# Kernel optimization log

Hardware: AMD Instinct MI355X
Metric: run time of the kernel (lower is better)

Reference implementation:

```python
import jax, jax.numpy as jnp
import numpy as np

N_STEPS = 5
DT = 0.1
# radius fixed from initial sigma = 0.5 + 4.5*sigmoid(0.5) = 3.301 -> ceil(3*sigma) = 10
RADIUS = 10
SIZE = 2 * RADIUS + 1


def _pad1(x):
    return jnp.pad(x, ((0, 0), (0, 0), (1, 1), (1, 1)), mode='reflect')


def _spatial_gradient(x):
    p = _pad1(x)
    gy = (p[:, :, 2:, 1:-1] - p[:, :, :-2, 1:-1]) / 2.0
    gx = (p[:, :, 1:-1, 2:] - p[:, :, 1:-1, :-2]) / 2.0
    return gy, gx


def _laplacian(x):
    p = _pad1(x)
    return (p[:, :, :-2, 1:-1] + p[:, :, 2:, 1:-1]
            + p[:, :, 1:-1, :-2] + p[:, :, 1:-1, 2:] - 4.0 * x)


def _gaussian_blur(x, sigma):
    # differentiable kernel weights, fixed size (matches torch: radius from detached sigma)
    coords = jnp.arange(SIZE, dtype=x.dtype) - RADIUS
    k = jnp.exp(-coords ** 2 / (2.0 * sigma ** 2 + 1e-8))
    k = k / (k.sum() + 1e-8)
    xp = jnp.pad(x, ((0, 0), (0, 0), (0, 0), (RADIUS, RADIUS)), mode='reflect')
    out = jax.lax.conv_general_dilated(xp, k.reshape(1, 1, 1, SIZE), (1, 1), 'VALID')
    out = jnp.pad(out, ((0, 0), (0, 0), (RADIUS, RADIUS), (0, 0)), mode='reflect')
    out = jax.lax.conv_general_dilated(out, k.reshape(1, 1, SIZE, 1), (1, 1), 'VALID')
    return out


def _forward(image, lfd_map, alpha_raw, lambda_raw, log_sigma, log_beta, log_xi,
             eta_raw, nu_raw, log_gamma, omega_raw):
    sig = jax.nn.sigmoid
    alpha = 0.6 + 1.4 * sig(alpha_raw)
    lam = 0.01 + 0.19 * sig(lambda_raw)
    sigma = 0.5 + 4.5 * sig(log_sigma)
    beta = 1.0 + 4.0 * sig(log_beta)
    xi = 1.0 + 4.0 * sig(log_xi)
    eta = sig(eta_raw)
    nu = sig(nu_raw)
    gamma = 1.0 + 3.0 * sig(log_gamma)
    omega = sig(omega_raw)

    fractal_weight = jnp.clip(1.0 - omega * lfd_map, 0.0, 1.0)  # (B,1,H,W)
    u = image
    u0 = image
    for _ in range(N_STEPS):
        u_sigma = _gaussian_blur(u, sigma)
        gy, gx = _spatial_gradient(u)
        gys, gxs = _spatial_gradient(u_sigma)
        grad_mag = jnp.sqrt(gx ** 2 + gy ** 2 + 1e-8)
        grad_mag_s = jnp.sqrt(gxs ** 2 + gys ** 2 + 1e-8)
        lap_abs = jnp.abs(_laplacian(u))
        # conductance phi(s) = beta*sqrt(xi/(eta*s^2+eps)), clamped at 10
        phi = jnp.minimum(beta * jnp.sqrt(xi / (eta * grad_mag_s ** 2 + 1e-6)), 10.0)
        phi_f = phi * fractal_weight
        # curvature modulation psi'(s) = 1e-4*sqrt(nu*s^3+gamma), s = |grad u|*|lap u|
        s = grad_mag * lap_abs
        psi = 1e-4 * jnp.sqrt(nu * s ** 3 + gamma)
        pu = _pad1(u)
        dn = pu[:, :, :-2, 1:-1] - u
        dso = pu[:, :, 2:, 1:-1] - u
        de = pu[:, :, 1:-1, 2:] - u
        dw = pu[:, :, 1:-1, :-2] - u
        pp = _pad1(phi_f)
        div = (pp[:, :, :-2, 1:-1] * dn + pp[:, :, 2:, 1:-1] * dso
               + pp[:, :, 1:-1, 2:] * de + pp[:, :, 1:-1, :-2] * dw)
        du = alpha * psi * div - lam * (u - u0)
        u = jnp.clip(u + DT * du, 0.0, 1.0)
    edge_residual = jnp.abs(image - u)
    er_max = edge_residual.max(axis=(-2, -1), keepdims=True)
    edge_residual = edge_residual / (er_max + 1e-8)
    return u, edge_residual


def setup_inputs() -> dict:
    key = jax.random.key(0)
    k1, k2 = jax.random.split(key)
    B, H, W = 16, 512, 512
    image = jax.random.uniform(k1, (B, 1, H, W), jnp.float32)
    lfd_map = jax.random.uniform(k2, (B, 1, H, W), jnp.float32)
    f = lambda v: jnp.asarray(v, jnp.float32)
    return {
        'image': image, 'lfd_map': lfd_map,
        'alpha_raw': f(0.0), 'lambda_raw': f(-2.0), 'log_sigma': f(0.5),
        'log_beta': f(0.5), 'log_xi': f(0.5), 'eta_raw': f(0.3),
        'nu_raw': f(0.0), 'log_gamma': f(0.5), 'omega_raw': f(0.5),
    }


def reference(image, lfd_map, alpha_raw, lambda_raw, log_sigma, log_beta, log_xi,
              eta_raw, nu_raw, log_gamma, omega_raw):
    return _forward(image, lfd_map, alpha_raw, lambda_raw, log_sigma, log_beta,
                    log_xi, eta_raw, nu_raw, log_gamma, omega_raw)
```

## Files before the change

kernel.cpp:

```cpp
#include <hip/hip_runtime.h>
#include <math.h>

#define HH 512
#define WW 512
#define NPIX (16*HH*WW)
#define RAD 10
#define KS 21
#define TX 64
#define TY 32
#define SH 42
#define SW 74
#define SSTR 90

__device__ __forceinline__ int refl(int v, int n){ v = v < 0 ? -v : v; return v >= n ? 2*n - 2 - v : v; }
__device__ __forceinline__ float sigm(float x){ return 1.f/(1.f+expf(-x)); }

__global__ void k_params(const float* a_raw, const float* l_raw, const float* lsig,
                         const float* lbeta, const float* lxi, const float* e_raw,
                         const float* n_raw, const float* lgam, const float* o_raw,
                         float* P)
{
    if (threadIdx.x || blockIdx.x) return;
    float sigma = 0.5f + 4.5f*sigm(lsig[0]);
    float beta  = 1.f + 4.f*sigm(lbeta[0]);
    float xi    = 1.f + 4.f*sigm(lxi[0]);
    float eta   = sigm(e_raw[0]);
    P[0] = 0.6f + 1.4f*sigm(a_raw[0]);
    P[1] = 0.01f + 0.19f*sigm(l_raw[0]);
    P[2] = beta;
    P[3] = xi;
    P[4] = eta;
    P[5] = sigm(n_raw[0]);
    P[6] = 1.f + 3.f*sigm(lgam[0]);
    P[7] = sigm(o_raw[0]);
    float kk[KS], s = 0.f;
    for (int i = 0; i < KS; ++i){ float c = (float)(i-RAD); kk[i] = expf(-c*c/(2.f*sigma*sigma+1e-8f)); s += kk[i]; }
    float inv = 1.f/(s+1e-8f);
    for (int i = 0; i < KS; ++i) P[8+i] = kk[i]*inv;
    P[30] = (beta*beta*xi >= 100.f*(eta*0.5000002f + 1e-6f)) ? 1.f : 0.f;
    for (int i = 0; i < 16; ++i) P[64+32*i] = 0.f;
}

#define ROW6(v, S, off) float v##0=(S)[(off)], v##1=(S)[(off)+1], v##2=(S)[(off)+2], \
                              v##3=(S)[(off)+3], v##4=(S)[(off)+4], v##5=(S)[(off)+5];
#define ROW8S(v, S, off) float v##m=(S)[(off)-2], v##0=(S)[(off)], v##1=(S)[(off)+1], v##2=(S)[(off)+2], \
                               v##3=(S)[(off)+3], v##4=(S)[(off)+4], v##5=(S)[(off)+5], v##6=(S)[(off)+7];

__global__ __launch_bounds__(256) __attribute__((amdgpu_waves_per_eu(4, 4)))
void k_mega(const float* __restrict__ img, const float* __restrict__ lfd,
            float* __restrict__ out_u, float* __restrict__ out_r,
            const float* __restrict__ P, float* Pmax)
{
    if (P[30] == 0.f) return;
    __shared__ float SA[SH*SSTR];
    __shared__ float SB[SH*SSTR];
    __shared__ float red[4];
    const int tid = threadIdx.x;
    const bool active = tid < 240;
    const int py = tid / 12;
    const int px = tid - 12*py;
    const int ox = blockIdx.x * TX, oy = blockIdx.y * TY;
    const int b = blockIdx.z;
    const float* ib = img + (b<<18);
    const float* lb = lfd + (b<<18);
    const float A = 1e-3f*P[0], lam = P[1], nu = P[5], gam = P[6], omg = P[7];
    const float nuA = A*A*nu, gamA = A*A*gam;
    const bool bord = (ox == 0) | (oy == 0) | (ox == WW - TX) | (oy == HH - TY);

    for (int i = tid; i < SW*SH; i += 256){
        int r = i / SW, c = i - r*SW;
        int gy = oy - 5 + r, gx = ox - 5 + c;
        if (bord){ gy = refl(gy, HH); gx = refl(gx, WW); }
        int gi = gy*WW + gx;
        int pc = (c == 0) ? 0 : (c + (c-1)/6 + 1);
        SA[r*SSTR + pc] = ib[gi];
        SB[r*SSTR + pc] = fminf(fmaxf(1.f - omg*lb[gi], 0.f), 1.f);
    }
    __syncthreads();

    const int c0 = 1 + 6*px;
    const int r0 = 1 + 2*py;
    const int bi = r0*SSTR + 7*px + 2;

    ROW6(fa, SB, bi-SSTR) ROW8S(fb, SB, bi) ROW8S(fc, SB, bi+SSTR) ROW6(fd, SB, bi+2*SSTR)
    ROW6(zb, SA, bi) ROW6(zc, SA, bi+SSTR)
    __syncthreads();

    float ub0=zb0, ub1=zb1, ub2=zb2, ub3=zb3, ub4=zb4, ub5=zb5;
    float uc0=zc0, uc1=zc1, uc2=zc2, uc3=zc3, uc4=zc4, uc5=zc5;

    auto CF = [&](float cc, float cn, float cs, float cw, float ce,
                  float fn, float fs, float fw_, float fe, float z) -> float {
        float dy = cs - cn, dx = ce - cw;
        float g2 = fmaf(0.25f, fmaf(dy, dy, dx*dx), 1e-8f);
        float t1 = (cn + cs) + (ce + cw);
        float lap = fmaf(-4.f, cc, t1);
        float s = sqrtf(g2) * fabsf(lap);
        float psiA = sqrtf(fmaf(nuA, s*s*s, gamA));
        float dv = fn*(cn-cc) + fs*(cs-cc) + fe*(ce-cc) + fw_*(cw-cc);
        float du = fmaf(psiA, dv, -lam*(cc - z));
        return fminf(fmaxf(fmaf(0.1f, du, cc), 0.f), 1.f);
    };

#define READ_HALO(S) \
    ROW6(ua, S, bi-SSTR) ROW6(ud, S, bi+2*SSTR) \
    float ubm=(S)[bi-2], ub6=(S)[bi+7], ucm=(S)[bi+SSTR-2], uc6=(S)[bi+SSTR+7];

#define CELLS \
    float nb0 = CF(ub0, ua0, uc0, ubm, ub1, fa0, fc0, fbm, fb1, zb0); \
    float nb1 = CF(ub1, ua1, uc1, ub0, ub2, fa1, fc1, fb0, fb2, zb1); \
    float nb2 = CF(ub2, ua2, uc2, ub1, ub3, fa2, fc2, fb1, fb3, zb2); \
    float nb3 = CF(ub3, ua3, uc3, ub2, ub4, fa3, fc3, fb2, fb4, zb3); \
    float nb4 = CF(ub4, ua4, uc4, ub3, ub5, fa4, fc4, fb3, fb5, zb4); \
    float nb5 = CF(ub5, ua5, uc5, ub4, ub6, fa5, fc5, fb4, fb6, zb5); \
    float nc0 = CF(uc0, ub0, ud0, ucm, uc1, fb0, fd0, fcm, fc1, zc0); \
    float nc1 = CF(uc1, ub1, ud1, uc0, uc2, fb1, fd1, fc0, fc2, zc1); \
    float nc2 = CF(uc2, ub2, ud2, uc1, uc3, fb2, fd2, fc1, fc3, zc2); \
    float nc3 = CF(uc3, ub3, ud3, uc2, uc4, fb3, fd3, fc2, fc4, zc3); \
    float nc4 = CF(uc4, ub4, ud4, uc3, uc5, fb4, fd4, fc3, fc5, zc4); \
    float nc5 = CF(uc5, ub5, ud5, uc4, uc6, fb5, fd5, fc4, fc6, zc5);

#define STEP(S, D) { \
    READ_HALO(S) \
    CELLS \
    if (active){ \
        D[bi]   = nb0; D[bi+1] = nb1; D[bi+2] = nb2; D[bi+3] = nb3; D[bi+4] = nb4; D[bi+5] = nb5; \
        D[bi+SSTR]   = nc0; D[bi+SSTR+1] = nc1; D[bi+SSTR+2] = nc2; \
        D[bi+SSTR+3] = nc3; D[bi+SSTR+4] = nc4; D[bi+SSTR+5] = nc5; \
    } \
    ub0=nb0; ub1=nb1; ub2=nb2; ub3=nb3; ub4=nb4; ub5=nb5; \
    uc0=nc0; uc1=nc1; uc2=nc2; uc3=nc3; uc4=nc4; uc5=nc5; \
    } __syncthreads();

    STEP(SA, SB)
    STEP(SB, SA)
    STEP(SA, SB)
    STEP(SB, SA)

    float mymax = 0.f;
    {
        READ_HALO(SA)
        CELLS
        if (active && py >= 2 && py <= 17){
            float* ou  = out_u + (b<<18) + (oy + r0 - 5)*WW + (ox + c0 - 5);
            float* orr = out_r + (b<<18) + (oy + r0 - 5)*WW + (ox + c0 - 5);
#define EMIT(K, NB, NC, ZB, ZC) \
            if (c0 + K >= 5 && c0 + K <= 68){ \
                ou[K] = NB; ou[WW + K] = NC; \
                float vb = fabsf(ZB - NB), vc = fabsf(ZC - NC); \
                orr[K] = vb; orr[WW + K] = vc; \
                mymax = fmaxf(mymax, fmaxf(vb, vc)); \
            }
            EMIT(0, nb0, nc0, zb0, zc0)
            EMIT(1, nb1, nc1, zb1, zc1)
            EMIT(2, nb2, nc2, zb2, zc2)
            EMIT(3, nb3, nc3, zb3, zc3)
            EMIT(4, nb4, nc4, zb4, zc4)
            EMIT(5, nb5, nc5, zb5, zc5)
#undef EMIT
        }
    }
#undef STEP
#undef CELLS
#undef READ_HALO

#pragma unroll
    for (int off = 32; off; off >>= 1) mymax = fmaxf(mymax, __shfl_down(mymax, off));
    if ((tid & 63) == 0) red[tid >> 6] = mymax;
    __syncthreads();
    if (tid == 0){
        float m = fmaxf(fmaxf(red[0], red[1]), fmaxf(red[2], red[3]));
        atomicMax((unsigned int*)(Pmax + 32*b), __float_as_uint(m));
    }
}

__global__ __launch_bounds__(256)
void k_iter(const float* __restrict__ src, const float* __restrict__ img,
            const float* __restrict__ lfd, float* __restrict__ dst,
            float* __restrict__ resid,
            const float* __restrict__ P, float* Pmax, int do_max)
{
    if (P[30] != 0.f) return;
    __shared__ __attribute__((aligned(16))) float sh[56][72];
    __shared__ float su[36][72];
    __shared__ float ut[34][72];
    __shared__ float red[4];
    float (*pt)[72] = sh;

    const int tid = threadIdx.x;
    const int x0 = blockIdx.x * TX;
    const int y0 = blockIdx.y * TY;
    const int b  = blockIdx.z;
    const float* sb = src + (b << 18);
    const float* ib = img + (b << 18);
    const float* lb = lfd + (b << 18);
    float* db = dst + (b << 18);

    float kw[KS];
#pragma unroll
    for (int j = 0; j < KS; ++j) kw[j] = P[8 + j];
    const float alpha = P[0], lam = P[1], beta = P[2], xi = P[3];
    const float eta = P[4], nu = P[5], gam = P[6], omg = P[7];

#pragma unroll
    for (int p = 0; p < 9; ++p) {
        int i = tid + p * 256;
        if (i < 34 * 66) {
            int r = i / 66, c = i - r * 66;
            ut[r][c] = sb[refl(y0 - 1 + r, HH) * WW + refl(x0 - 1 + c, WW)];
        }
    }
#pragma unroll
    for (int p = 0; p < 4; ++p) {
        int i = tid + p * 256;
        if (i < 56 * 17) {
            int hr = i / 17, g = i - hr * 17;
            const float* row = sb + refl(y0 - 12 + hr, HH) * WW;
            int gxs = x0 - 12 + 4 * g;
            float wv[24];
            if (gxs >= 0 && gxs + 23 < WW) {
                const float4* p4 = (const float4*)(row + gxs);
#pragma unroll
                for (int q = 0; q < 6; ++q) {
                    float4 v = p4[q];
                    wv[4*q] = v.x; wv[4*q+1] = v.y; wv[4*q+2] = v.z; wv[4*q+3] = v.w;
                }
            } else {
#pragma unroll
                for (int q = 0; q < 24; ++q) wv[q] = row[refl(gxs + q, WW)];
            }
            float a0 = 0.f, a1 = 0.f, a2 = 0.f, a3 = 0.f;
#pragma unroll
            for (int j = 0; j < KS; ++j) {
                a0 = fmaf(kw[j], wv[j],     a0);
                a1 = fmaf(kw[j], wv[j + 1], a1);
                a2 = fmaf(kw[j], wv[j + 2], a2);
                a3 = fmaf(kw[j], wv[j + 3], a3);
            }
            float4 o; o.x = a0; o.y = a1; o.z = a2; o.w = a3;
            *(float4*)&sh[hr][4 * g] = o;
        }
    }
    __syncthreads();
#pragma unroll
    for (int p = 0; p < 3; ++p) {
        int i = tid + p * 256;
        if (i < 9 * 68) {
            int rg = i / 68, c = i - rg * 68;
            int r0 = rg * 4;
            float a0 = 0.f, a1 = 0.f, a2 = 0.f, a3 = 0.f;
#pragma unroll
            for (int q = 0; q < 24; ++q) {
                float s = sh[r0 + q][c];
                if (q <= 20)           a0 = fmaf(kw[q],     s, a0);
                if (q >= 1 && q <= 21) a1 = fmaf(kw[q - 1], s, a1);
                if (q >= 2 && q <= 22) a2 = fmaf(kw[q - 2], s, a2);
                if (q >= 3)            a3 = fmaf(kw[q - 3], s, a3);
            }
            su[r0][c] = a0; su[r0+1][c] = a1; su[r0+2][c] = a2; su[r0+3][c] = a3;
        }
    }
    __syncthreads();
#pragma unroll
    for (int p = 0; p < 9; ++p) {
        int i = tid + p * 256;
        if (i < 34 * 66) {
            int r = i / 66, c = i - r * 66;
            float gys = (su[r + 2][c + 1] - su[r][c + 1]) * 0.5f;
            float gxs = (su[r + 1][c + 2] - su[r + 1][c]) * 0.5f;
            float g2 = fmaf(gxs, gxs, fmaf(gys, gys, 1e-8f));
            float ph = fminf(beta * sqrtf(xi / fmaf(eta, g2, 1e-6f)), 10.f);
            float lv = lb[refl(y0 - 1 + r, HH) * WW + refl(x0 - 1 + c, WW)];
            float fwv = fminf(fmaxf(1.f - omg * lv, 0.f), 1.f);
            pt[r][c] = ph * fwv;
        }
    }
    __syncthreads();
    const int c = tid & 63, r0 = tid >> 6;
    float mymax = 0.f;
#pragma unroll
    for (int p = 0; p < 8; ++p) {
        int r = r0 + p * 4;
        float uc = ut[r + 1][c + 1];
        float uN = ut[r][c + 1],     uS = ut[r + 2][c + 1];
        float uE = ut[r + 1][c + 2], uW = ut[r + 1][c];
        float gy = (uS - uN) * 0.5f, gx = (uE - uW) * 0.5f;
        float lap = uN + uS + uE + uW - 4.f * uc;
        float gm = sqrtf(fmaf(gx, gx, fmaf(gy, gy, 1e-8f)));
        float s = gm * fabsf(lap);
        float psi = 1e-4f * sqrtf(fmaf(nu, s * s * s, gam));
        float pN = pt[r][c + 1],     pS = pt[r + 2][c + 1];
        float pE = pt[r + 1][c + 2], pW = pt[r + 1][c];
        float dv = pN * (uN - uc) + pS * (uS - uc) + pE * (uE - uc) + pW * (uW - uc);
        int gidx = (y0 + r) * WW + x0 + c;
        float u0v = ib[gidx];
        float du = alpha * psi * dv - lam * (uc - u0v);
        float un = fminf(fmaxf(fmaf(0.1f, du, uc), 0.f), 1.f);
        db[gidx] = un;
        if (do_max){
            float v = fabsf(u0v - un);
            resid[(b<<18) + gidx] = v;
            mymax = fmaxf(mymax, v);
        }
    }
    if (do_max) {
#pragma unroll
        for (int off = 32; off; off >>= 1) mymax = fmaxf(mymax, __shfl_down(mymax, off));
        if ((tid & 63) == 0) red[tid >> 6] = mymax;
        __syncthreads();
        if (tid == 0) {
            float m = fmaxf(fmaxf(red[0], red[1]), fmaxf(red[2], red[3]));
            atomicMax((unsigned int*)(Pmax + 32 * b), __float_as_uint(m));
        }
    }
}

__global__ void k_res2(float* __restrict__ r, const float* __restrict__ Pmax)
{
    int i = blockIdx.x * 256 + threadIdx.x;
    int b = i >> 16;
    float inv = 1.f / (Pmax[32 * b] + 1e-8f);
    float4 v = ((const float4*)r)[i];
    v.x *= inv; v.y *= inv; v.z *= inv; v.w *= inv;
    ((float4*)r)[i] = v;
}

extern "C" void kernel_launch(void* const* d_in, const int* in_sizes, int n_in,
                              void* d_out, int out_size, void* d_ws, size_t ws_size,
                              hipStream_t stream)
{
    const float* image = (const float*)d_in[0];
    const float* lfd   = (const float*)d_in[1];

    float* out_u = (float*)d_out;
    float* out_r = out_u + NPIX;

    float* uB = (float*)d_ws;
    float* P  = uB + NPIX;

    k_params<<<1, 64, 0, stream>>>((const float*)d_in[2], (const float*)d_in[3],
                                   (const float*)d_in[4], (const float*)d_in[5],
                                   (const float*)d_in[6], (const float*)d_in[7],
                                   (const float*)d_in[8], (const float*)d_in[9],
                                   (const float*)d_in[10], P);

    float* Pmax = P + 64;

    dim3 grd(WW/TX, HH/TY, 16), blk(256);
    k_mega<<<grd, blk, 0, stream>>>(image, lfd, out_u, out_r, P, Pmax);

    float* bufs[2] = { out_u, uB };
    for (int it = 0; it < 5; ++it) {
        const float* src = (it == 0) ? image : bufs[(it + 1) & 1];
        float* dstp = bufs[it & 1];
        k_iter<<<grd, blk, 0, stream>>>(src, image, lfd, dstp, out_r, P, Pmax, it == 4 ? 1 : 0);
    }

    k_res2<<<NPIX/1024, 256, 0, stream>>>(out_r, Pmax);
}
```

Measured before the change: 82.57 us.

## Inline parameter computation, drop atomics, recompute residual in final normalize pass

Removes the single-thread k_params launch by recomputing the scalar parameters (and the Gaussian taps in k_iter) inside each kernel. The per-batch atomicMax is replaced by per-block max slots that k_res2 reduces itself, which also removes the need to zero Pmax. The residual is no longer written by the main kernels; k_res2 recomputes |image-u| and normalizes it, trading a residual store plus reload for an extra read of image and u. The waves-per-eu hint on k_mega is loosened to a minimum of 5.

```diff
diff --git a/kernel.cpp b/kernel.cpp
--- a/kernel.cpp
+++ b/kernel.cpp
@@ -15,43 +15,31 @@
 __device__ __forceinline__ int refl(int v, int n){ v = v < 0 ? -v : v; return v >= n ? 2*n - 2 - v : v; }
 __device__ __forceinline__ float sigm(float x){ return 1.f/(1.f+expf(-x)); }
 
-__global__ void k_params(const float* a_raw, const float* l_raw, const float* lsig,
-                         const float* lbeta, const float* lxi, const float* e_raw,
-                         const float* n_raw, const float* lgam, const float* o_raw,
-                         float* P)
-{
-    if (threadIdx.x || blockIdx.x) return;
-    float sigma = 0.5f + 4.5f*sigm(lsig[0]);
-    float beta  = 1.f + 4.f*sigm(lbeta[0]);
-    float xi    = 1.f + 4.f*sigm(lxi[0]);
-    float eta   = sigm(e_raw[0]);
-    P[0] = 0.6f + 1.4f*sigm(a_raw[0]);
-    P[1] = 0.01f + 0.19f*sigm(l_raw[0]);
-    P[2] = beta;
-    P[3] = xi;
-    P[4] = eta;
-    P[5] = sigm(n_raw[0]);
-    P[6] = 1.f + 3.f*sigm(lgam[0]);
-    P[7] = sigm(o_raw[0]);
-    float kk[KS], s = 0.f;
-    for (int i = 0; i < KS; ++i){ float c = (float)(i-RAD); kk[i] = expf(-c*c/(2.f*sigma*sigma+1e-8f)); s += kk[i]; }
-    float inv = 1.f/(s+1e-8f);
-    for (int i = 0; i < KS; ++i) P[8+i] = kk[i]*inv;
-    P[30] = (beta*beta*xi >= 100.f*(eta*0.5000002f + 1e-6f)) ? 1.f : 0.f;
-    for (int i = 0; i < 16; ++i) P[64+32*i] = 0.f;
-}
+#define PARAMS_PRELUDE \
+    const float alpha = 0.6f + 1.4f*sigm(a_raw[0]); \
+    const float lam   = 0.01f + 0.19f*sigm(l_raw[0]); \
+    const float beta  = 1.f + 4.f*sigm(lbeta[0]); \
+    const float xi    = 1.f + 4.f*sigm(lxi[0]); \
+    const float eta   = sigm(e_raw[0]); \
+    const float nu    = sigm(n_raw[0]); \
+    const float gam   = 1.f + 3.f*sigm(lgam[0]); \
+    const float omg   = sigm(o_raw[0]); \
+    const bool  sat   = (beta*beta*xi >= 100.f*(eta*0.5000002f + 1e-6f));
 
 #define ROW6(v, S, off) float v##0=(S)[(off)], v##1=(S)[(off)+1], v##2=(S)[(off)+2], \
                               v##3=(S)[(off)+3], v##4=(S)[(off)+4], v##5=(S)[(off)+5];
 #define ROW8S(v, S, off) float v##m=(S)[(off)-2], v##0=(S)[(off)], v##1=(S)[(off)+1], v##2=(S)[(off)+2], \
                                v##3=(S)[(off)+3], v##4=(S)[(off)+4], v##5=(S)[(off)+5], v##6=(S)[(off)+7];
 
-__global__ __launch_bounds__(256) __attribute__((amdgpu_waves_per_eu(4, 4)))
+__global__ __launch_bounds__(256) __attribute__((amdgpu_waves_per_eu(5)))
 void k_mega(const float* __restrict__ img, const float* __restrict__ lfd,
-            float* __restrict__ out_u, float* __restrict__ out_r,
-            const float* __restrict__ P, float* Pmax)
+            float* __restrict__ out_u, float* __restrict__ slots,
+            const float* a_raw, const float* l_raw, const float* lbeta,
+            const float* lxi, const float* e_raw, const float* n_raw,
+            const float* lgam, const float* o_raw)
 {
-    if (P[30] == 0.f) return;
+    PARAMS_PRELUDE
+    if (!sat) return;
     __shared__ float SA[SH*SSTR];
     __shared__ float SB[SH*SSTR];
     __shared__ float red[4];
@@ -63,7 +51,7 @@
     const int b = blockIdx.z;
     const float* ib = img + (b<<18);
     const float* lb = lfd + (b<<18);
-    const float A = 1e-3f*P[0], lam = P[1], nu = P[5], gam = P[6], omg = P[7];
+    const float A = 1e-3f*alpha;
     const float nuA = A*A*nu, gamA = A*A*gam;
     const bool bord = (ox == 0) | (oy == 0) | (ox == WW - TX) | (oy == HH - TY);
 
@@ -142,14 +130,11 @@
         READ_HALO(SA)
         CELLS
         if (active && py >= 2 && py <= 17){
-            float* ou  = out_u + (b<<18) + (oy + r0 - 5)*WW + (ox + c0 - 5);
-            float* orr = out_r + (b<<18) + (oy + r0 - 5)*WW + (ox + c0 - 5);
+            float* ou = out_u + (b<<18) + (oy + r0 - 5)*WW + (ox + c0 - 5);
 #define EMIT(K, NB, NC, ZB, ZC) \
             if (c0 + K >= 5 && c0 + K <= 68){ \
                 ou[K] = NB; ou[WW + K] = NC; \
-                float vb = fabsf(ZB - NB), vc = fabsf(ZC - NC); \
-                orr[K] = vb; orr[WW + K] = vc; \
-                mymax = fmaxf(mymax, fmaxf(vb, vc)); \
+                mymax = fmaxf(mymax, fmaxf(fabsf(ZB - NB), fabsf(ZC - NC))); \
             }
             EMIT(0, nb0, nc0, zb0, zc0)
             EMIT(1, nb1, nc1, zb1, zc1)
@@ -170,17 +155,35 @@
     __syncthreads();
     if (tid == 0){
         float m = fmaxf(fmaxf(red[0], red[1]), fmaxf(red[2], red[3]));
-        atomicMax((unsigned int*)(Pmax + 32*b), __float_as_uint(m));
+        slots[(b<<7) + blockIdx.y*8 + blockIdx.x] = m;
     }
 }
 
 __global__ __launch_bounds__(256)
 void k_iter(const float* __restrict__ src, const float* __restrict__ img,
             const float* __restrict__ lfd, float* __restrict__ dst,
-            float* __restrict__ resid,
-            const float* __restrict__ P, float* Pmax, int do_max)
+            float* __restrict__ slots, int do_max,
+            const float* a_raw, const float* l_raw, const float* lsig,
+            const float* lbeta, const float* lxi, const float* e_raw,
+            const float* n_raw, const float* lgam, const float* o_raw)
 {
-    if (P[30] != 0.f) return;
+    PARAMS_PRELUDE
+    if (sat) return;
+    const float sigma = 0.5f + 4.5f*sigm(lsig[0]);
+    float kw[KS];
+    {
+        float s = 0.f;
+#pragma unroll
+        for (int i = 0; i < KS; ++i){
+            float c = (float)(i - RAD);
+            kw[i] = expf(-c*c/(2.f*sigma*sigma + 1e-8f));
+            s += kw[i];
+        }
+        float inv = 1.f/(s + 1e-8f);
+#pragma unroll
+        for (int i = 0; i < KS; ++i) kw[i] *= inv;
+    }
+
     __shared__ __attribute__((aligned(16))) float sh[56][72];
     __shared__ float su[36][72];
     __shared__ float ut[34][72];
@@ -195,12 +198,6 @@
     const float* ib = img + (b << 18);
     const float* lb = lfd + (b << 18);
     float* db = dst + (b << 18);
-
-    float kw[KS];
-#pragma unroll
-    for (int j = 0; j < KS; ++j) kw[j] = P[8 + j];
-    const float alpha = P[0], lam = P[1], beta = P[2], xi = P[3];
-    const float eta = P[4], nu = P[5], gam = P[6], omg = P[7];
 
 #pragma unroll
     for (int p = 0; p < 9; ++p) {
@@ -297,11 +294,7 @@
         float du = alpha * psi * dv - lam * (uc - u0v);
         float un = fminf(fmaxf(fmaf(0.1f, du, uc), 0.f), 1.f);
         db[gidx] = un;
-        if (do_max){
-            float v = fabsf(u0v - un);
-            resid[(b<<18) + gidx] = v;
-            mymax = fmaxf(mymax, v);
-        }
+        mymax = fmaxf(mymax, fabsf(u0v - un));
     }
     if (do_max) {
 #pragma unroll
@@ -310,19 +303,40 @@
         __syncthreads();
         if (tid == 0) {
             float m = fmaxf(fmaxf(red[0], red[1]), fmaxf(red[2], red[3]));
-            atomicMax((unsigned int*)(Pmax + 32 * b), __float_as_uint(m));
+            slots[(b << 7) + blockIdx.y*8 + blockIdx.x] = m;
         }
     }
 }
 
-__global__ void k_res2(float* __restrict__ r, const float* __restrict__ Pmax)
+__global__ __launch_bounds__(256)
+void k_res2(const float* __restrict__ img, const float* __restrict__ u,
+            float* __restrict__ r, const float* __restrict__ slots)
 {
-    int i = blockIdx.x * 256 + threadIdx.x;
-    int b = i >> 16;
-    float inv = 1.f / (Pmax[32 * b] + 1e-8f);
-    float4 v = ((const float4*)r)[i];
-    v.x *= inv; v.y *= inv; v.z *= inv; v.w *= inv;
-    ((float4*)r)[i] = v;
+    __shared__ float sm[2];
+    const int tid = threadIdx.x;
+    const int blk = blockIdx.x;
+    const int b = blk >> 6;
+    float m = 0.f;
+    if (tid < 128) m = slots[(b << 7) + tid];
+#pragma unroll
+    for (int off = 32; off; off >>= 1) m = fmaxf(m, __shfl_down(m, off));
+    if (tid == 0)  sm[0] = m;
+    if (tid == 64) sm[1] = m;
+    __syncthreads();
+    const float inv = 1.f / (fmaxf(sm[0], sm[1]) + 1e-8f);
+    const int base = blk * 1024 + tid;
+#pragma unroll
+    for (int k = 0; k < 4; ++k){
+        int i = base + k * 256;
+        float4 a = ((const float4*)img)[i];
+        float4 c = ((const float4*)u)[i];
+        float4 o;
+        o.x = fabsf(a.x - c.x) * inv;
+        o.y = fabsf(a.y - c.y) * inv;
+        o.z = fabsf(a.z - c.z) * inv;
+        o.w = fabsf(a.w - c.w) * inv;
+        ((float4*)r)[i] = o;
+    }
 }
 
 extern "C" void kernel_launch(void* const* d_in, const int* in_sizes, int n_in,
@@ -331,30 +345,34 @@
 {
     const float* image = (const float*)d_in[0];
     const float* lfd   = (const float*)d_in[1];
+    const float* a_raw = (const float*)d_in[2];
+    const float* l_raw = (const float*)d_in[3];
+    const float* lsig  = (const float*)d_in[4];
+    const float* lbeta = (const float*)d_in[5];
+    const float* lxi   = (const float*)d_in[6];
+    const float* e_raw = (const float*)d_in[7];
+    const float* n_raw = (const float*)d_in[8];
+    const float* lgam  = (const float*)d_in[9];
+    const float* o_raw = (const float*)d_in[10];
 
     float* out_u = (float*)d_out;
     float* out_r = out_u + NPIX;
 
-    float* uB = (float*)d_ws;
-    float* P  = uB + NPIX;
-
-    k_params<<<1, 64, 0, stream>>>((const float*)d_in[2], (const float*)d_in[3],
-                                   (const float*)d_in[4], (const float*)d_in[5],
-                                   (const float*)d_in[6], (const float*)d_in[7],
-                                   (const float*)d_in[8], (const float*)d_in[9],
-                                   (const float*)d_in[10], P);
-
-    float* Pmax = P + 64;
+    float* uB    = (float*)d_ws;
+    float* slots = uB + NPIX;
 
     dim3 grd(WW/TX, HH/TY, 16), blk(256);
-    k_mega<<<grd, blk, 0, stream>>>(image, lfd, out_u, out_r, P, Pmax);
+
+    k_mega<<<grd, blk, 0, stream>>>(image, lfd, out_u, slots,
+                                    a_raw, l_raw, lbeta, lxi, e_raw, n_raw, lgam, o_raw);
 
     float* bufs[2] = { out_u, uB };
     for (int it = 0; it < 5; ++it) {
         const float* src = (it == 0) ? image : bufs[(it + 1) & 1];
         float* dstp = bufs[it & 1];
-        k_iter<<<grd, blk, 0, stream>>>(src, image, lfd, dstp, out_r, P, Pmax, it == 4 ? 1 : 0);
-    }
-
-    k_res2<<<NPIX/1024, 256, 0, stream>>>(out_r, Pmax);
+        k_iter<<<grd, blk, 0, stream>>>(src, image, lfd, dstp, slots, it == 4 ? 1 : 0,
+                                        a_raw, l_raw, lsig, lbeta, lxi, e_raw, n_raw, lgam, o_raw);
+    }
+
+    k_res2<<<1024, 256, 0, stream>>>(image, out_u, out_r, slots);
 }
```

Result: no change. 81.06 us (-1.8%).
